# Kernel optimization log

Hardware: AMD Instinct MI355X
Metric: run time of the kernel (lower is better)

The kernel has to match this reference:

```python
import jax, jax.numpy as jnp
import numpy as np


def setup_inputs() -> dict:
    key = jax.random.key(0)
    ks = jax.random.split(key, 9)
    b, m, e, d = 4, 4096, 2048, 256
    s = 1.0 / np.sqrt(d)
    return {
        "features": jax.random.normal(ks[0], (b, m, d), jnp.float32),
        "inc_mat": (jax.random.uniform(ks[1], (b, m, e)) < 0.05).astype(jnp.float32),
        "vc_W_att": jax.random.normal(ks[2], (d, d), jnp.float32) * s,
        "vc_W_proj": jax.random.normal(ks[3], (d, d), jnp.float32) * s,
        "vc_alpha": jnp.float32(0.5),
        "ec_W_att": jax.random.normal(ks[4], (d, d), jnp.float32) * s,
        "ec_W_proj": jax.random.normal(ks[5], (d, d), jnp.float32) * s,
        "ec_alpha": jnp.float32(0.5),
        "n_layers": 3,
    }


def _vertex_conv(feat, inc, W_att, W_proj, alpha, prev_edge):
    # feat: [b,m,d], inc: [b,m,e]
    node_scores = jnp.einsum('bmd,kd->bmk', feat, W_att)          # attention Linear (x @ W.T)
    edge_scores = jnp.einsum('bme,bmd->bed', inc, node_scores)    # inc^T @ scores
    attn = jax.nn.softmax(edge_scores, axis=1)                    # softmax over edge dim (dim=1 in torch)
    # einsum('bme,bmd->bmed') then ('bmed,bed->bed') == attn * (inc^T @ feat); no 4D intermediate
    agg = jnp.einsum('bme,bmd->bed', inc, feat)
    ef = jnp.einsum('bed,kd->bek', attn * agg, W_proj)
    if prev_edge is not None:
        ef = alpha * prev_edge + (1.0 - alpha) * ef
    return ef


def _edge_conv(inc, edge_feats, W_proj, alpha, prev_node):
    # note: EdgeConv's attention softmax is computed but unused in the original forward
    weighted = jnp.einsum('bed,bme->bmd', edge_feats, inc)        # scatter edges back to nodes
    nf = jnp.einsum('bmd,kd->bmk', weighted, W_proj)
    if prev_node is not None:
        nf = alpha * prev_node + (1.0 - alpha) * nf
    return nf


def reference(features, inc_mat, vc_W_att, vc_W_proj, vc_alpha, ec_W_att, ec_W_proj, ec_alpha, n_layers):
    edge_feats = _vertex_conv(features, inc_mat, vc_W_att, vc_W_proj, vc_alpha, None)
    node_feats = _edge_conv(inc_mat, edge_feats, ec_W_proj, ec_alpha, features)
    for _ in range(1, int(n_layers)):
        edge_feats = _vertex_conv(features, inc_mat, vc_W_att, vc_W_proj, vc_alpha, edge_feats)
        node_feats = _edge_conv(inc_mat, edge_feats, ec_W_proj, ec_alpha, node_feats)
    return (node_feats, edge_feats, inc_mat)
```

## Files before the change

### kernel.cpp

```cpp
#include <hip/hip_runtime.h>
#include <hip/hip_bf16.h>
#include <math.h>

typedef __attribute__((ext_vector_type(8))) short s8v;
typedef __attribute__((ext_vector_type(4))) float f32x4;

__device__ __forceinline__ ushort f2bf(float x){ __hip_bfloat16 h = __float2bfloat16(x); return *(ushort*)&h; }
__device__ __forceinline__ float  bf2f(ushort u){ return __bfloat162float(*(__hip_bfloat16*)&u); }

template<int MAP> __device__ __forceinline__ int kmap(int k){
  if constexpr (MAP==0) return k;
  else if constexpr (MAP==1) return k & 4095;
  else if constexpr (MAP==3) return (((k>>8)&1)<<8) | (k&255);
  else if constexpr (MAP==4) return k & 255;
  else return (((k>>9)&1)<<8) | (k&255);
}

template<int AMAP, int BMAP, int EPI, int FR>
__global__ __launch_bounds__(256)
void gemm_kernel(const ushort* __restrict__ A, int lda, long long sA,
                 const ushort* __restrict__ B, int ldb, long long sB,
                 void* __restrict__ Cp, void* __restrict__ Cp2,
                 int ldc, long long sC, int ldc2, long long sC2,
                 long long kpC, int Kloc, int kparts,
                 const float* __restrict__ blend,
                 const float* __restrict__ alpha_p, const int* __restrict__ L_p)
{
  constexpr int BMt = 32*FR;
  __shared__ ushort As[BMt][40];
  __shared__ ushort Bs[BMt][40];

  const int z  = blockIdx.z;
  const int b  = z / kparts;
  const int kp = z - b*kparts;
  const int kbase = kp * Kloc;
  A += (size_t)b * sA;
  B += (size_t)b * sB;
  const int m0 = blockIdx.x * BMt;
  const int n0 = blockIdx.y * BMt;
  const int t = threadIdx.x, lane = t & 63, wid = t >> 6;
  const int wr = (wid>>1)*(16*FR), wc = (wid&1)*(16*FR);
  const int lrow = lane & 15, koff = (lane>>4)<<3;

  f32x4 acc[FR][FR];
  #pragma unroll
  for (int i=0;i<FR;i++)
    #pragma unroll
    for (int j=0;j<FR;j++) acc[i][j] = (f32x4)(0.f);

  for (int k0 = 0; k0 < Kloc; k0 += 32) {
    if constexpr (FR==4) {
      const int row = t>>1, cb = (t&1)*16;
      { const ushort* s = A + (size_t)(m0+row)*lda + kmap<AMAP>(kbase+k0+cb);
        *(s8v*)&As[row][cb] = *(const s8v*)s; *(s8v*)&As[row][cb+8] = *(const s8v*)(s+8); }
      { const ushort* s = B + (size_t)(n0+row)*ldb + kmap<BMAP>(kbase+k0+cb);
        *(s8v*)&Bs[row][cb] = *(const s8v*)s; *(s8v*)&Bs[row][cb+8] = *(const s8v*)(s+8); }
    } else {
      const int row = t>>2, cb = (t&3)*8;
      *(s8v*)&As[row][cb] = *(const s8v*)(A + (size_t)(m0+row)*lda + kmap<AMAP>(kbase+k0+cb));
      *(s8v*)&Bs[row][cb] = *(const s8v*)(B + (size_t)(n0+row)*ldb + kmap<BMAP>(kbase+k0+cb));
    }
    __syncthreads();
    s8v af[FR], bfv[FR];
    #pragma unroll
    for (int mi=0; mi<FR; mi++) af[mi]  = *(const s8v*)&As[wr+mi*16+lrow][koff];
    #pragma unroll
    for (int ni=0; ni<FR; ni++) bfv[ni] = *(const s8v*)&Bs[wc+ni*16+lrow][koff];
    #pragma unroll
    for (int mi=0; mi<FR; mi++)
      #pragma unroll
      for (int ni=0; ni<FR; ni++)
        acc[mi][ni] = __builtin_amdgcn_mfma_f32_16x16x32_bf16(af[mi], bfv[ni], acc[mi][ni], 0,0,0);
    __syncthreads();
  }

  float aL = 0.f;
  if constexpr (EPI==2) { aL = powf(*alpha_p, (float)(*L_p)); }
  const int cr = (lane>>4)<<2, cc = lane & 15;
  #pragma unroll
  for (int mi=0; mi<FR; mi++)
    #pragma unroll
    for (int ni=0; ni<FR; ni++) {
      const int row0 = m0 + wr + mi*16 + cr;
      const int col  = n0 + wc + ni*16 + cc;
      if constexpr (EPI==0) {
        float* C = (float*)Cp + kp*kpC + (size_t)b*sC;
        #pragma unroll
        for (int r=0;r<4;r++) C[(size_t)(row0+r)*ldc + col] = acc[mi][ni][r];
      } else if constexpr (EPI==1) {
        ushort* C = (ushort*)Cp + (size_t)b*sC;
        #pragma unroll
        for (int r=0;r<4;r++) C[(size_t)(row0+r)*ldc + col] = f2bf(acc[mi][ni][r]);
      } else if constexpr (EPI==2) {
        float* C = (float*)Cp + (size_t)b*sC;
        const float* bl = blend + (size_t)b*sC;
        #pragma unroll
        for (int r=0;r<4;r++) {
          const size_t idx = (size_t)(row0+r)*ldc + col;
          C[idx] = aL*bl[idx] + (1.f-aL)*acc[mi][ni][r];
        }
      } else if constexpr (EPI==6) {
        float* C = (float*)Cp + (size_t)b*sC;
        #pragma unroll
        for (int r=0;r<4;r++) C[(size_t)(row0+r)*ldc + col] = acc[mi][ni][r];
        float* C2 = (float*)Cp2 + (size_t)b*sC2 + (size_t)col*ldc2 + row0;
        *(f32x4*)C2 = acc[mi][ni];
      } else {
        float* C = (float*)Cp + (size_t)b*sC;
        #pragma unroll
        for (int r=0;r<4;r++) C[(size_t)(row0+r)*ldc + col] = acc[mi][ni][r];
        ushort4 o;
        o.x = f2bf(acc[mi][ni][0]); o.y = f2bf(acc[mi][ni][1]);
        o.z = f2bf(acc[mi][ni][2]); o.w = f2bf(acc[mi][ni][3]);
        *(ushort4*)((ushort*)Cp2 + (size_t)b*sC2 + (size_t)col*ldc2 + row0) = o;
      }
    }
}

__global__ __launch_bounds__(256)
void trans_inc_kernel(const float* __restrict__ src, float* __restrict__ outF32, int writeF32,
                      ushort* __restrict__ incbf, ushort* __restrict__ incT)
{
  __shared__ ushort T[64][65];
  const int b = blockIdx.z, m0 = blockIdx.x*64, e0 = blockIdx.y*64;
  const int t = threadIdx.x, rl = t>>2, cl = (t&3)*16;
  const size_t roff = (size_t)b*4096*2048 + (size_t)(m0+rl)*2048 + e0 + cl;
  const float* s = src + roff;
  ushort tmp[16] __attribute__((aligned(16)));
  float4 vv[4];
  #pragma unroll
  for (int i=0;i<4;i++) {
    vv[i] = ((const float4*)s)[i];
    tmp[4*i+0]=f2bf(vv[i].x); tmp[4*i+1]=f2bf(vv[i].y);
    tmp[4*i+2]=f2bf(vv[i].z); tmp[4*i+3]=f2bf(vv[i].w);
  }
  if (writeF32) {
    float4* o = (float4*)(outF32 + roff);
    #pragma unroll
    for (int i=0;i<4;i++) o[i] = vv[i];
  }
  ushort* d = incbf + roff;
  *(s8v*)d = *(s8v*)&tmp[0]; *(s8v*)(d+8) = *(s8v*)&tmp[8];
  #pragma unroll
  for (int j=0;j<16;j++) T[rl][cl+j] = tmp[j];
  __syncthreads();
  const int er = t>>2, mc = (t&3)*16;
  ushort o[16] __attribute__((aligned(16)));
  #pragma unroll
  for (int j=0;j<16;j++) o[j] = T[mc+j][er];
  ushort* d2 = incT + (size_t)b*2048*4096 + (size_t)(e0+er)*4096 + m0 + mc;
  *(s8v*)d2 = *(s8v*)&o[0]; *(s8v*)(d2+8) = *(s8v*)&o[8];
}

__global__ __launch_bounds__(256)
void trans_feat_kernel(const float* __restrict__ feat, ushort* __restrict__ fT)
{
  __shared__ ushort Th[64][65], Tl[64][65];
  const int b = blockIdx.z, m0 = blockIdx.x*64, d0 = blockIdx.y*64;
  const int t = threadIdx.x, rl = t>>2, cl = (t&3)*16;
  const float* s = feat + (size_t)b*4096*256 + (size_t)(m0+rl)*256 + d0 + cl;
  #pragma unroll
  for (int i=0;i<4;i++) {
    float4 v = ((const float4*)s)[i];
    float a[4] = {v.x,v.y,v.z,v.w};
    #pragma unroll
    for (int j=0;j<4;j++) {
      ushort h = f2bf(a[j]); Th[rl][cl+4*i+j] = h; Tl[rl][cl+4*i+j] = f2bf(a[j] - bf2f(h));
    }
  }
  __syncthreads();
  const int dr = t>>2, mc = (t&3)*16;
  ushort oh[16] __attribute__((aligned(16)));
  ushort ol[16] __attribute__((aligned(16)));
  #pragma unroll
  for (int j=0;j<16;j++) { oh[j] = Th[mc+j][dr]; ol[j] = Tl[mc+j][dr]; }
  ushort* d2 = fT + (size_t)b*256*8192 + (size_t)(d0+dr)*8192 + m0 + mc;
  *(s8v*)d2 = *(s8v*)&oh[0]; *(s8v*)(d2+8) = *(s8v*)&oh[8];
  *(s8v*)(d2+4096) = *(s8v*)&ol[0]; *(s8v*)(d2+4104) = *(s8v*)&ol[8];
}

__global__ __launch_bounds__(256)
void cvt_w_kernel(const float4* __restrict__ W, ushort* __restrict__ Ws)
{
  size_t i  = (size_t)blockIdx.x * 256 + threadIdx.x;
  size_t e0 = i * 4;
  int c = (int)(e0 & 255), r = (int)(e0 >> 8);
  float4 v = W[i];
  float a[4] = {v.x,v.y,v.z,v.w};
  ushort* hi = Ws + (size_t)r*512 + c;
  #pragma unroll
  for (int j=0;j<4;j++) { ushort h = f2bf(a[j]); hi[j] = h; hi[256+j] = f2bf(a[j]-bf2f(h)); }
}

__global__ __launch_bounds__(256)
void aggsum_kernel(const float* __restrict__ parts, long long kpC, int kparts,
                   ushort* __restrict__ AGGcat)
{
  const size_t i4 = (size_t)blockIdx.x*256 + threadIdx.x;
  float4 sv = make_float4(0.f,0.f,0.f,0.f);
  for (int kp=0; kp<kparts; kp++) {
    float4 v = ((const float4*)(parts + (size_t)kp*kpC))[i4];
    sv.x+=v.x; sv.y+=v.y; sv.z+=v.z; sv.w+=v.w;
  }
  const size_t flat = i4*4;
  const size_t row = flat >> 8;
  const int d = (int)(flat & 255);
  float a[4] = {sv.x, sv.y, sv.z, sv.w};
  ushort4 hi, lo;
  { ushort h=f2bf(a[0]); hi.x=h; lo.x=f2bf(a[0]-bf2f(h)); }
  { ushort h=f2bf(a[1]); hi.y=h; lo.y=f2bf(a[1]-bf2f(h)); }
  { ushort h=f2bf(a[2]); hi.z=h; lo.z=f2bf(a[2]-bf2f(h)); }
  { ushort h=f2bf(a[3]); hi.w=h; lo.w=f2bf(a[3]-bf2f(h)); }
  ushort* dst = AGGcat + row*512 + d;
  *(ushort4*)dst = hi; *(ushort4*)(dst+256) = lo;
}

__global__ __launch_bounds__(256)
void stats_kernel(const float* __restrict__ ESt, float2* __restrict__ stats)
{
  const int b = blockIdx.x >> 8, d = blockIdx.x & 255;
  const float* base = ESt + ((size_t)b*256 + d)*2048;
  const int t = threadIdx.x;
  const float4* p = (const float4*)base + t*2;
  float4 x = p[0], y = p[1];
  float v[8] = {x.x,x.y,x.z,x.w,y.x,y.y,y.z,y.w};
  float mx = v[0];
  #pragma unroll
  for (int j=1;j<8;j++) mx = fmaxf(mx, v[j]);
  #pragma unroll
  for (int off=32; off>=1; off>>=1) mx = fmaxf(mx, __shfl_down(mx, off));
  __shared__ float sm[8];
  const int lane = t & 63, w = t >> 6;
  if (lane==0) sm[w] = mx;
  __syncthreads();
  if (t==0) { sm[4] = fmaxf(fmaxf(sm[0],sm[1]),fmaxf(sm[2],sm[3])); }
  __syncthreads();
  mx = sm[4];
  float s = 0.f;
  #pragma unroll
  for (int j=0;j<8;j++) s += __expf(v[j]-mx);
  #pragma unroll
  for (int off=32; off>=1; off>>=1) s += __shfl_down(s, off);
  if (lane==0) sm[w] = s;
  __syncthreads();
  if (t==0) { float ss = sm[0]+sm[1]+sm[2]+sm[3]; stats[blockIdx.x] = make_float2(mx, 1.f/ss); }
}

__global__ __launch_bounds__(256)
void pmul_kernel(const float* __restrict__ ES, const ushort* __restrict__ AGGcat,
                 const float2* __restrict__ stats, ushort* __restrict__ P)
{
  const int b = blockIdx.x >> 6, e0 = (blockIdx.x & 63) * 32;
  const int t = threadIdx.x, tx = t & 63, ty = t >> 6;
  const int d4 = tx*4;
  const float2 st0 = stats[b*256+d4+0], st1 = stats[b*256+d4+1];
  const float2 st2 = stats[b*256+d4+2], st3 = stats[b*256+d4+3];
  for (int e = e0+ty; e < e0+32; e += 4) {
    const size_t ro = (size_t)b*2048 + e;
    float4 es = *(const float4*)(ES + ro*256 + d4);
    ushort4 ah = *(const ushort4*)(AGGcat + ro*512 + d4);
    ushort4 al = *(const ushort4*)(AGGcat + ro*512 + 256 + d4);
    ushort4 o;
    o.x = f2bf(__expf(es.x-st0.x)*st0.y*(bf2f(ah.x)+bf2f(al.x)));
    o.y = f2bf(__expf(es.y-st1.x)*st1.y*(bf2f(ah.y)+bf2f(al.y)));
    o.z = f2bf(__expf(es.z-st2.x)*st2.y*(bf2f(ah.z)+bf2f(al.z)));
    o.w = f2bf(__expf(es.w-st3.x)*st3.y*(bf2f(ah.w)+bf2f(al.w)));
    *(ushort4*)(P + ro*256 + d4) = o;
  }
}

__global__ __launch_bounds__(256)
void inc_copy_kernel(const float4* __restrict__ src, float4* __restrict__ dst, size_t n4)
{
  size_t i = (size_t)blockIdx.x*256 + threadIdx.x;
  const size_t stride = (size_t)gridDim.x*256;
  for (; i < n4; i += stride) dst[i] = src[i];
}

extern "C" void kernel_launch(void* const* d_in, const int* in_sizes, int n_in,
                              void* d_out, int out_size, void* d_ws, size_t ws_size,
                              hipStream_t stream) {
  const float* feat    = (const float*)d_in[0];
  const float* inc     = (const float*)d_in[1];
  const float* vcWatt  = (const float*)d_in[2];
  const float* vcWproj = (const float*)d_in[3];
  const float* ecWproj = (const float*)d_in[6];
  const float* ecAlpha = (const float*)d_in[7];
  const int*   nLayers = (const int*)d_in[8];

  const int Bb=4, Mm=4096, E=2048, D=256;
  const size_t nodeN = (size_t)Bb*Mm*D, edgeN = (size_t)Bb*E*D, incN = (size_t)Bb*Mm*E;

  const int kparts = 8;
  const size_t fTB    = (size_t)Bb*256*8192*2;
  const size_t partsB = (size_t)kparts*Bb*E*D*4;
  const size_t AGGcatB= (size_t)Bb*E*512*2;
  const size_t ESB    = (size_t)Bb*E*D*4;
  const size_t EStB   = ESB;
  const size_t PB     = edgeN*2;
  const size_t edgeTB = edgeN*2;
  const size_t WtB    = nodeN*2;
  const size_t WsB    = (size_t)3*256*512*2;
  const size_t statB  = (size_t)Bb*256*sizeof(float2);
  const size_t incTB  = incN*2, incbfB = incN*2;
  const size_t needB  = fTB+partsB+AGGcatB+ESB+EStB+PB+edgeTB+WtB+WsB+statB;
  const bool planA = ws_size >= needB + incTB + incbfB;

  char* ws = (char*)d_ws;
  ushort* fT    = (ushort*)ws;  ws += fTB;
  float*  parts = (float*)ws;   ws += partsB;
  ushort* AGGcat= (ushort*)ws;  ws += AGGcatB;
  float*  ES    = (float*)ws;   ws += ESB;
  float*  ESt   = (float*)ws;   ws += EStB;
  ushort* P     = (ushort*)ws;  ws += PB;
  ushort* edgeT = (ushort*)ws;  ws += edgeTB;
  ushort* Wt    = (ushort*)ws;  ws += WtB;
  ushort* Ws0   = (ushort*)ws;
  ushort* Ws1   = Ws0 + 256*512;
  ushort* Ws2   = Ws1 + 256*512;
  ws += WsB;
  float2* stats = (float2*)ws;  ws += statB;

  float* outNode = (float*)d_out;
  float* outEdge = outNode + nodeN;
  float* outInc  = outEdge + edgeN;
  ushort* incT, *incbf;
  if (planA) { incT = (ushort*)ws; incbf = incT + incN; }
  else       { incT = (ushort*)outInc; incbf = incT + incN; }

  const long long kpC = (long long)Bb*E*D;
  dim3 blk(256);

  cvt_w_kernel<<<dim3(64), blk, 0, stream>>>((const float4*)vcWatt,  Ws0);
  cvt_w_kernel<<<dim3(64), blk, 0, stream>>>((const float4*)vcWproj, Ws1);
  cvt_w_kernel<<<dim3(64), blk, 0, stream>>>((const float4*)ecWproj, Ws2);
  trans_feat_kernel<<<dim3(64,4,4), blk, 0, stream>>>(feat, fT);
  trans_inc_kernel<<<dim3(64,32,4), blk, 0, stream>>>(inc, outInc, planA ? 1 : 0, incbf, incT);

  gemm_kernel<1,0,0,4><<<dim3(16,2,4*kparts), blk, 0, stream>>>(
      incT, 4096, (long long)E*4096, fT, 8192, (long long)256*8192,
      parts, nullptr, D, (long long)E*D, 0, 0, kpC, 8192/kparts, kparts,
      nullptr, nullptr, nullptr);

  aggsum_kernel<<<dim3(2048), blk, 0, stream>>>(parts, kpC, kparts, AGGcat);

  gemm_kernel<5,3,6,2><<<dim3(32,4,4), blk, 0, stream>>>(
      AGGcat, 512, (long long)E*512, Ws0, 512, 0,
      ES, ESt, D, (long long)E*D, E, (long long)D*E, 0, 1024, 1,
      nullptr, nullptr, nullptr);

  stats_kernel<<<dim3(Bb*256), blk, 0, stream>>>(ESt, stats);
  pmul_kernel<<<dim3(Bb*64), blk, 0, stream>>>(ES, AGGcat, stats, P);

  gemm_kernel<4,3,7,2><<<dim3(32,4,4), blk, 0, stream>>>(
      P, 256, (long long)E*D, Ws1, 512, 0,
      outEdge, edgeT, D, (long long)E*D, E, (long long)D*E, 0, 512, 1,
      nullptr, nullptr, nullptr);

  gemm_kernel<0,0,1,2><<<dim3(64,4,4), blk, 0, stream>>>(
      incbf, 2048, (long long)Mm*E, edgeT, 2048, (long long)D*E,
      Wt, nullptr, D, (long long)Mm*D, 0, 0, 0, 2048, 1,
      nullptr, nullptr, nullptr);

  gemm_kernel<4,3,2,2><<<dim3(64,4,4), blk, 0, stream>>>(
      Wt, 256, (long long)Mm*D, Ws2, 512, 0,
      outNode, nullptr, D, (long long)Mm*D, 0, 0, 0, 512, 1,
      feat, ecAlpha, nLayers);

  if (!planA)
    inc_copy_kernel<<<dim3(2048), blk, 0, stream>>>((const float4*)inc, (float4*)outInc, incN/4);
}
```

Before: 527.5 us.

## Use direct global-to-LDS loads, nontemporal streaming stores, and swapped grid order

```diff
diff --git a/kernel.cpp b/kernel.cpp
--- a/kernel.cpp
+++ b/kernel.cpp
@@ -7,6 +7,12 @@
 
 __device__ __forceinline__ ushort f2bf(float x){ __hip_bfloat16 h = __float2bfloat16(x); return *(ushort*)&h; }
 __device__ __forceinline__ float  bf2f(ushort u){ return __bfloat162float(*(__hip_bfloat16*)&u); }
+
+__device__ __forceinline__ void gload16(const void* g, void* l) {
+  __builtin_amdgcn_global_load_lds(
+      (const __attribute__((address_space(1))) void*)g,
+      (__attribute__((address_space(3))) void*)l, 16, 0, 0);
+}
 
 template<int MAP> __device__ __forceinline__ int kmap(int k){
   if constexpr (MAP==0) return k;
@@ -27,8 +33,8 @@
                  const float* __restrict__ alpha_p, const int* __restrict__ L_p)
 {
   constexpr int BMt = 32*FR;
-  __shared__ ushort As[BMt][40];
-  __shared__ ushort Bs[BMt][40];
+  __shared__ ushort As[BMt][32];
+  __shared__ ushort Bs[BMt][32];
 
   const int z  = blockIdx.z;
   const int b  = z / kparts;
@@ -36,11 +42,13 @@
   const int kbase = kp * Kloc;
   A += (size_t)b * sA;
   B += (size_t)b * sB;
-  const int m0 = blockIdx.x * BMt;
-  const int n0 = blockIdx.y * BMt;
+  const int m0 = blockIdx.y * BMt;
+  const int n0 = blockIdx.x * BMt;
   const int t = threadIdx.x, lane = t & 63, wid = t >> 6;
   const int wr = (wid>>1)*(16*FR), wc = (wid&1)*(16*FR);
   const int lrow = lane & 15, koff = (lane>>4)<<3;
+  const int rsub = lane >> 2;
+  const int kc   = (lane & 3) * 8;
 
   f32x4 acc[FR][FR];
   #pragma unroll
@@ -49,16 +57,11 @@
     for (int j=0;j<FR;j++) acc[i][j] = (f32x4)(0.f);
 
   for (int k0 = 0; k0 < Kloc; k0 += 32) {
-    if constexpr (FR==4) {
-      const int row = t>>1, cb = (t&1)*16;
-      { const ushort* s = A + (size_t)(m0+row)*lda + kmap<AMAP>(kbase+k0+cb);
-        *(s8v*)&As[row][cb] = *(const s8v*)s; *(s8v*)&As[row][cb+8] = *(const s8v*)(s+8); }
-      { const ushort* s = B + (size_t)(n0+row)*ldb + kmap<BMAP>(kbase+k0+cb);
-        *(s8v*)&Bs[row][cb] = *(const s8v*)s; *(s8v*)&Bs[row][cb+8] = *(const s8v*)(s+8); }
-    } else {
-      const int row = t>>2, cb = (t&3)*8;
-      *(s8v*)&As[row][cb] = *(const s8v*)(A + (size_t)(m0+row)*lda + kmap<AMAP>(kbase+k0+cb));
-      *(s8v*)&Bs[row][cb] = *(const s8v*)(B + (size_t)(n0+row)*ldb + kmap<BMAP>(kbase+k0+cb));
+    #pragma unroll
+    for (int c = wid; c < 2*FR; c += 4) {
+      const int row = c*16 + rsub;
+      gload16(A + (size_t)(m0+row)*lda + kmap<AMAP>(kbase+k0+kc), (char*)&As[0][0] + c*1024);
+      gload16(B + (size_t)(n0+row)*ldb + kmap<BMAP>(kbase+k0+kc), (char*)&Bs[0][0] + c*1024);
     }
     __syncthreads();
     s8v af[FR], bfv[FR];
@@ -127,20 +130,21 @@
   const size_t roff = (size_t)b*4096*2048 + (size_t)(m0+rl)*2048 + e0 + cl;
   const float* s = src + roff;
   ushort tmp[16] __attribute__((aligned(16)));
-  float4 vv[4];
+  f32x4 vv[4];
   #pragma unroll
   for (int i=0;i<4;i++) {
-    vv[i] = ((const float4*)s)[i];
-    tmp[4*i+0]=f2bf(vv[i].x); tmp[4*i+1]=f2bf(vv[i].y);
-    tmp[4*i+2]=f2bf(vv[i].z); tmp[4*i+3]=f2bf(vv[i].w);
+    vv[i] = __builtin_nontemporal_load(((const f32x4*)s) + i);
+    tmp[4*i+0]=f2bf(vv[i][0]); tmp[4*i+1]=f2bf(vv[i][1]);
+    tmp[4*i+2]=f2bf(vv[i][2]); tmp[4*i+3]=f2bf(vv[i][3]);
   }
   if (writeF32) {
-    float4* o = (float4*)(outF32 + roff);
-    #pragma unroll
-    for (int i=0;i<4;i++) o[i] = vv[i];
+    f32x4* o = (f32x4*)(outF32 + roff);
+    #pragma unroll
+    for (int i=0;i<4;i++) __builtin_nontemporal_store(vv[i], o + i);
   }
   ushort* d = incbf + roff;
-  *(s8v*)d = *(s8v*)&tmp[0]; *(s8v*)(d+8) = *(s8v*)&tmp[8];
+  __builtin_nontemporal_store(*(s8v*)&tmp[0], (s8v*)d);
+  __builtin_nontemporal_store(*(s8v*)&tmp[8], (s8v*)(d+8));
   #pragma unroll
   for (int j=0;j<16;j++) T[rl][cl+j] = tmp[j];
   __syncthreads();
@@ -149,7 +153,8 @@
   #pragma unroll
   for (int j=0;j<16;j++) o[j] = T[mc+j][er];
   ushort* d2 = incT + (size_t)b*2048*4096 + (size_t)(e0+er)*4096 + m0 + mc;
-  *(s8v*)d2 = *(s8v*)&o[0]; *(s8v*)(d2+8) = *(s8v*)&o[8];
+  __builtin_nontemporal_store(*(s8v*)&o[0], (s8v*)d2);
+  __builtin_nontemporal_store(*(s8v*)&o[8], (s8v*)(d2+8));
 }
 
 __global__ __launch_bounds__(256)
@@ -270,11 +275,12 @@
 }
 
 __global__ __launch_bounds__(256)
-void inc_copy_kernel(const float4* __restrict__ src, float4* __restrict__ dst, size_t n4)
+void inc_copy_kernel(const f32x4* __restrict__ src, f32x4* __restrict__ dst, size_t n4)
 {
   size_t i = (size_t)blockIdx.x*256 + threadIdx.x;
   const size_t stride = (size_t)gridDim.x*256;
-  for (; i < n4; i += stride) dst[i] = src[i];
+  for (; i < n4; i += stride)
+    __builtin_nontemporal_store(__builtin_nontemporal_load(src + i), dst + i);
 }
 
 extern "C" void kernel_launch(void* const* d_in, const int* in_sizes, int n_in,
@@ -337,14 +343,14 @@
   trans_feat_kernel<<<dim3(64,4,4), blk, 0, stream>>>(feat, fT);
   trans_inc_kernel<<<dim3(64,32,4), blk, 0, stream>>>(inc, outInc, planA ? 1 : 0, incbf, incT);
 
-  gemm_kernel<1,0,0,4><<<dim3(16,2,4*kparts), blk, 0, stream>>>(
+  gemm_kernel<1,0,0,4><<<dim3(2,16,4*kparts), blk, 0, stream>>>(
       incT, 4096, (long long)E*4096, fT, 8192, (long long)256*8192,
       parts, nullptr, D, (long long)E*D, 0, 0, kpC, 8192/kparts, kparts,
       nullptr, nullptr, nullptr);
 
   aggsum_kernel<<<dim3(2048), blk, 0, stream>>>(parts, kpC, kparts, AGGcat);
 
-  gemm_kernel<5,3,6,2><<<dim3(32,4,4), blk, 0, stream>>>(
+  gemm_kernel<5,3,6,2><<<dim3(4,32,4), blk, 0, stream>>>(
       AGGcat, 512, (long long)E*512, Ws0, 512, 0,
       ES, ESt, D, (long long)E*D, E, (long long)D*E, 0, 1024, 1,
       nullptr, nullptr, nullptr);
@@ -352,21 +358,21 @@
   stats_kernel<<<dim3(Bb*256), blk, 0, stream>>>(ESt, stats);
   pmul_kernel<<<dim3(Bb*64), blk, 0, stream>>>(ES, AGGcat, stats, P);
 
-  gemm_kernel<4,3,7,2><<<dim3(32,4,4), blk, 0, stream>>>(
+  gemm_kernel<4,3,7,2><<<dim3(4,32,4), blk, 0, stream>>>(
       P, 256, (long long)E*D, Ws1, 512, 0,
       outEdge, edgeT, D, (long long)E*D, E, (long long)D*E, 0, 512, 1,
       nullptr, nullptr, nullptr);
 
-  gemm_kernel<0,0,1,2><<<dim3(64,4,4), blk, 0, stream>>>(
+  gemm_kernel<0,0,1,2><<<dim3(4,64,4), blk, 0, stream>>>(
       incbf, 2048, (long long)Mm*E, edgeT, 2048, (long long)D*E,
       Wt, nullptr, D, (long long)Mm*D, 0, 0, 0, 2048, 1,
       nullptr, nullptr, nullptr);
 
-  gemm_kernel<4,3,2,2><<<dim3(64,4,4), blk, 0, stream>>>(
+  gemm_kernel<4,3,2,2><<<dim3(4,64,4), blk, 0, stream>>>(
       Wt, 256, (long long)Mm*D, Ws2, 512, 0,
       outNode, nullptr, D, (long long)Mm*D, 0, 0, 0, 512, 1,
       feat, ecAlpha, nLayers);
 
   if (!planA)
-    inc_copy_kernel<<<dim3(2048), blk, 0, stream>>>((const float4*)inc, (float4*)outInc, incN/4);
-}
+    inc_copy_kernel<<<dim3(2048), blk, 0, stream>>>((const f32x4*)inc, (f32x4*)outInc, incN/4);
+}
```

Result: slower. 655.0 us (+24.2%).
